# Kernel optimization log

Hardware: AMD Instinct MI355X
Metric: run time of the kernel (lower is better)

Reference implementation:

```python
import jax, jax.numpy as jnp
import numpy as np

IN_SIZE = 128
H_UNITS = 256
REC_MAX = min(25.0, 1.0 / float(np.sqrt(H_UNITS)))  # clip bound for recurrent kernels


def setup_inputs() -> dict:
    key = jax.random.key(0)
    ks = jax.random.split(key, 8)
    B, T, D, U = 64, 4096, IN_SIZE, H_UNITS
    xs = jax.random.normal(ks[0], (B, T, D), dtype=jnp.float32)
    # Original code inits input kernels/biases to zeros (degenerate); use small
    # random values so the baseline exercises nontrivial math (same formula).
    We = jax.random.normal(ks[1], (U, D), dtype=jnp.float32) * 0.02
    be = jnp.zeros((U,), dtype=jnp.float32)
    ue = jax.random.uniform(ks[2], (U,), minval=-REC_MAX, maxval=REC_MAX, dtype=jnp.float32)
    Wd = jax.random.normal(ks[3], (U, D), dtype=jnp.float32) * 0.02
    bd = jnp.zeros((U,), dtype=jnp.float32)
    ud = jax.random.uniform(ks[4], (U,), minval=-REC_MAX, maxval=REC_MAX, dtype=jnp.float32)
    lim = 1.0 / float(np.sqrt(U))  # torch.nn.Linear default init bound
    Wo = jax.random.uniform(ks[5], (D, U), minval=-lim, maxval=lim, dtype=jnp.float32)
    bo = jax.random.uniform(ks[6], (D,), minval=-lim, maxval=lim, dtype=jnp.float32)
    return {"xs": xs, "We": We, "be": be, "ue": ue, "Wd": Wd, "bd": bd, "ud": ud, "Wo": Wo, "bo": bo}


def reference(xs, We, be, ue, Wd, bd, ud, Wo, bo):
    B, T, D = xs.shape
    ue_c = jnp.clip(ue, -REC_MAX, REC_MAX)
    ud_c = jnp.clip(ud, -REC_MAX, REC_MAX)
    # IndRNN.forward never updates self.h, so the encoder hidden state is zeros
    # at every timestep; the encoder loop reduces to its last iteration:
    h = jax.nn.relu(xs[:, -1] @ We.T + be + ue_c * 0.0)  # [B, U]
    # ys[0]: readout of the (fixed) decoder hidden state
    out0 = h @ Wo.T + bo  # [B, D]
    loss = (xs[:, -1] - out0) ** 2  # [B, D]
    # train_step: decoder h stays fixed at encoder h for every timestep ->
    # all T-1 steps vectorize over time.
    dec_h = jax.nn.relu(jnp.einsum('btd,ud->btu', xs[:, 1:], Wd) + bd + ud_c * h[:, None, :])  # [B,T-1,U]
    outs = jnp.einsum('btu,du->btd', dec_h, Wo) + bo  # [B,T-1,D]
    loss = loss + jnp.sum((xs[:, :-1] - outs) ** 2, axis=1)  # sum over reversed(range(1,T))
    loss = loss / T
    return jnp.sum(loss) / B
```

## Files before the change

### kernel.cpp

```cpp
#include <hip/hip_runtime.h>

#define T_LEN 4096
#define D_IN 128
#define U_H 256
#define REC_MAXV 0.0625f

typedef __attribute__((ext_vector_type(4))) float f32x4;
typedef __attribute__((ext_vector_type(16))) float f32x16;
typedef __attribute__((ext_vector_type(2))) int int2v;
typedef long long i64;

template <bool HI>
__device__ __forceinline__ int pk8(float a, float b, int old) {
    return __builtin_amdgcn_cvt_pk_fp8_f32(a, b, old, HI);
}

__device__ __forceinline__ int reord32(int u) {
    int r = u & 31;
    return ((u >> 5) << 5) + (((r >> 2) & 1) << 4) + ((r >> 3) << 2) + (r & 3);
}

__global__ void k_pre(const float* __restrict__ xs, const float* __restrict__ We,
                      const float* __restrict__ be, const float* __restrict__ Wd,
                      const float* __restrict__ bd, const float* __restrict__ ud,
                      const float* __restrict__ Wo, const float* __restrict__ bo,
                      float* __restrict__ budR, float* __restrict__ boR,
                      char* __restrict__ WF8, float* __restrict__ part2) {
    __shared__ __align__(16) float hL[256];
    __shared__ float red[2];
    const int b = blockIdx.x, u = threadIdx.x;

    const f32x4* xr = (const f32x4*)(xs + ((size_t)b * T_LEN + (T_LEN - 1)) * D_IN);
    const f32x4* wr = (const f32x4*)(We + (size_t)u * D_IN);
    float s = 0.f;
#pragma unroll
    for (int i = 0; i < 32; ++i) {
        f32x4 a = xr[i], w = wr[i];
        s += a[0]*w[0] + a[1]*w[1] + a[2]*w[2] + a[3]*w[3];
    }
    s += be[u];
    s = fmaxf(s, 0.f);
    hL[u] = s;

    float udc = fminf(fmaxf(ud[u], -REC_MAXV), REC_MAXV);
    budR[(b << 8) + reord32(u)] = bd[u] + udc * s;

    if (b == 0 && u < 128) boR[reord32(u)] = bo[u];

    int gid = b * 256 + u;
    if (gid < 4096) {
        int f = gid >> 6, l = gid & 63;
        int ut = f >> 3, ks = f & 7;
        const float* src = Wd + (size_t)(ut * 32 + (l & 31)) * D_IN + ks * 16 + (l >> 5) * 8;
        int lo = pk8<false>(src[0], src[1], 0); lo = pk8<true>(src[2], src[3], lo);
        int hh = pk8<false>(src[4], src[5], 0); hh = pk8<true>(src[6], src[7], hh);
        *(int2v*)(WF8 + (size_t)gid * 8) = (int2v){lo, hh};
    } else if (gid < 8192) {
        int g = gid - 4096;
        int f = g >> 6, l = g & 63;
        int uk = f >> 2, dt = f & 3;
        const float* src = Wo + (size_t)(dt * 32 + (l & 31)) * U_H + uk * 16 + (l >> 5) * 8;
        int lo = pk8<false>(src[0], src[1], 0); lo = pk8<true>(src[2], src[3], lo);
        int hh = pk8<false>(src[4], src[5], 0); hh = pk8<true>(src[6], src[7], hh);
        *(int2v*)(WF8 + 32768 + (size_t)g * 8) = (int2v){lo, hh};
    }
    __syncthreads();

    float v = 0.f;
    if (u < 128) {
        const f32x4* hr = (const f32x4*)hL;
        const f32x4* wo = (const f32x4*)(Wo + (size_t)u * U_H);
        float s2 = 0.f;
#pragma unroll
        for (int i = 0; i < 64; ++i) {
            f32x4 a = hr[i], w = wo[i];
            s2 += a[0]*w[0] + a[1]*w[1] + a[2]*w[2] + a[3]*w[3];
        }
        s2 += bo[u];
        float x = xs[((size_t)b * T_LEN + T_LEN - 1) * D_IN + u];
        float diff = x - s2;
        v = diff * diff;
    }
#pragma unroll
    for (int o = 32; o > 0; o >>= 1) v += __shfl_down(v, o);
    if (u == 0) red[0] = v;
    if (u == 64) red[1] = v;
    __syncthreads();
    if (u == 0) part2[b] = red[0] + red[1];
}

__global__ __launch_bounds__(512, 2) void k_main(
        const float* __restrict__ xs, const float* __restrict__ budR,
        const float* __restrict__ boR, const char* __restrict__ WF8,
        float* __restrict__ part) {
    __shared__ __align__(16) char lds[67200];
    const int tid = threadIdx.x;

    for (int i = tid; i < 4096; i += 512)
        ((f32x4*)lds)[i] = ((const f32x4*)WF8)[i];
    const int b = blockIdx.x >> 4;
    if (tid < 64) ((f32x4*)(lds + 65536))[tid] = ((const f32x4*)(budR + b * 256))[tid];
    else if (tid < 96) ((f32x4*)(lds + 66560))[tid - 64] = ((const f32x4*)boR)[tid - 64];
    __syncthreads();

    const int wave = tid >> 6, lane = tid & 63;
    const int m = lane & 31, hi = lane >> 5;
    const float* xsb = xs + ((size_t)b << 19);
    const float* budL = (const float*)(lds + 65536);
    const float* boL  = (const float*)(lds + 66560);
    float* wsumf = (float*)(lds + 67072);

    const int tile = blockIdx.x * 8 + wave;
    const int t0 = (tile & 127) << 5;

    const float* xrow = xsb + (size_t)(t0 + m) * 128 + hi * 8;
    i64 x0, x1, x2, x3, x4, x5, x6, x7;
    {
#define LDX(KS, XV)                                                      \
        {   f32x4 v0 = *(const f32x4*)(xrow + KS * 16);                  \
            f32x4 v1 = *(const f32x4*)(xrow + KS * 16 + 4);              \
            int lo = pk8<false>(v0[0], v0[1], 0); lo = pk8<true>(v0[2], v0[3], lo); \
            int hh = pk8<false>(v1[0], v1[1], 0); hh = pk8<true>(v1[2], v1[3], hh); \
            XV = __builtin_bit_cast(i64, (int2v){lo, hh}); }
        LDX(0, x0) LDX(1, x1) LDX(2, x2) LDX(3, x3)
        LDX(4, x4) LDX(5, x5) LDX(6, x6) LDX(7, x7)
#undef LDX
    }

    f32x16 o0, o1, o2, o3;
#define OINIT(OV, DT)                                                    \
    {   const float* bp = boL + (DT) * 32 + hi * 16;                     \
        f32x4 b0 = *(const f32x4*)(bp), b1 = *(const f32x4*)(bp + 4);    \
        f32x4 b2 = *(const f32x4*)(bp + 8), b3 = *(const f32x4*)(bp + 12); \
        OV[0]=b0[0]; OV[1]=b0[1]; OV[2]=b0[2]; OV[3]=b0[3];              \
        OV[4]=b1[0]; OV[5]=b1[1]; OV[6]=b1[2]; OV[7]=b1[3];              \
        OV[8]=b2[0]; OV[9]=b2[1]; OV[10]=b2[2]; OV[11]=b2[3];            \
        OV[12]=b3[0]; OV[13]=b3[1]; OV[14]=b3[2]; OV[15]=b3[3]; }
    OINIT(o0, 0) OINIT(o1, 1) OINIT(o2, 2) OINIT(o3, 3)
#undef OINIT

#pragma clang loop unroll(disable)
    for (int ut = 0; ut < 8; ++ut) {
        f32x16 ca, cb;
        {
            const float* bp = budL + ut * 32 + hi * 16;
            f32x4 b0 = *(const f32x4*)(bp), b1 = *(const f32x4*)(bp + 4);
            f32x4 b2 = *(const f32x4*)(bp + 8), b3 = *(const f32x4*)(bp + 12);
            ca[0]=b0[0]; ca[1]=b0[1]; ca[2]=b0[2]; ca[3]=b0[3];
            ca[4]=b1[0]; ca[5]=b1[1]; ca[6]=b1[2]; ca[7]=b1[3];
            ca[8]=b2[0]; ca[9]=b2[1]; ca[10]=b2[2]; ca[11]=b2[3];
            ca[12]=b3[0]; ca[13]=b3[1]; ca[14]=b3[2]; ca[15]=b3[3];
#pragma unroll
            for (int i = 0; i < 16; ++i) cb[i] = 0.f;
        }
        const char* wb = lds + ((ut * 8) << 9) + (lane << 3);
        ca = __builtin_amdgcn_mfma_f32_32x32x16_fp8_fp8(*(const i64*)(wb + 0*512), x0, ca, 0,0,0);
        cb = __builtin_amdgcn_mfma_f32_32x32x16_fp8_fp8(*(const i64*)(wb + 1*512), x1, cb, 0,0,0);
        ca = __builtin_amdgcn_mfma_f32_32x32x16_fp8_fp8(*(const i64*)(wb + 2*512), x2, ca, 0,0,0);
        cb = __builtin_amdgcn_mfma_f32_32x32x16_fp8_fp8(*(const i64*)(wb + 3*512), x3, cb, 0,0,0);
        ca = __builtin_amdgcn_mfma_f32_32x32x16_fp8_fp8(*(const i64*)(wb + 4*512), x4, ca, 0,0,0);
        cb = __builtin_amdgcn_mfma_f32_32x32x16_fp8_fp8(*(const i64*)(wb + 5*512), x5, cb, 0,0,0);
        ca = __builtin_amdgcn_mfma_f32_32x32x16_fp8_fp8(*(const i64*)(wb + 6*512), x6, ca, 0,0,0);
        cb = __builtin_amdgcn_mfma_f32_32x32x16_fp8_fp8(*(const i64*)(wb + 7*512), x7, cb, 0,0,0);

        i64 dlo, dhi;
        {
            f32x16 c;
#pragma unroll
            for (int i = 0; i < 16; ++i) c[i] = fmaxf(ca[i] + cb[i], 0.f);
            int d0 = pk8<false>(c[0],  c[1],  0); d0 = pk8<true>(c[2],  c[3],  d0);
            int d1 = pk8<false>(c[4],  c[5],  0); d1 = pk8<true>(c[6],  c[7],  d1);
            int d2 = pk8<false>(c[8],  c[9],  0); d2 = pk8<true>(c[10], c[11], d2);
            int d3 = pk8<false>(c[12], c[13], 0); d3 = pk8<true>(c[14], c[15], d3);
            int2v s = __builtin_amdgcn_permlane32_swap(d0, d1, false, false);
            int2v t = __builtin_amdgcn_permlane32_swap(d2, d3, false, false);
            dlo = __builtin_bit_cast(i64, s);
            dhi = __builtin_bit_cast(i64, t);
        }

        const char* w2 = lds + 32768 + ((ut * 8) << 9) + (lane << 3);
        o0 = __builtin_amdgcn_mfma_f32_32x32x16_fp8_fp8(*(const i64*)(w2 + 0*512), dlo, o0, 0,0,0);
        o1 = __builtin_amdgcn_mfma_f32_32x32x16_fp8_fp8(*(const i64*)(w2 + 1*512), dlo, o1, 0,0,0);
        o2 = __builtin_amdgcn_mfma_f32_32x32x16_fp8_fp8(*(const i64*)(w2 + 2*512), dlo, o2, 0,0,0);
        o3 = __builtin_amdgcn_mfma_f32_32x32x16_fp8_fp8(*(const i64*)(w2 + 3*512), dlo, o3, 0,0,0);
        o0 = __builtin_amdgcn_mfma_f32_32x32x16_fp8_fp8(*(const i64*)(w2 + 4*512), dhi, o0, 0,0,0);
        o1 = __builtin_amdgcn_mfma_f32_32x32x16_fp8_fp8(*(const i64*)(w2 + 5*512), dhi, o1, 0,0,0);
        o2 = __builtin_amdgcn_mfma_f32_32x32x16_fp8_fp8(*(const i64*)(w2 + 6*512), dhi, o2, 0,0,0);
        o3 = __builtin_amdgcn_mfma_f32_32x32x16_fp8_fp8(*(const i64*)(w2 + 7*512), dhi, o3, 0,0,0);
    }

    const int t = t0 + m;
    const float sel = (t > 0) ? 1.f : 0.f;
    const float* trow = xsb + (size_t)((t > 0) ? t - 1 : 0) * 128;
    float lacc = 0.f;
#define EPI(OV, DT)                                                      \
    {   _Pragma("unroll")                                                \
        for (int q = 0; q < 4; ++q) {                                    \
            f32x4 tg = *(const f32x4*)(trow + (DT) * 32 + q * 8 + hi * 4); \
            _Pragma("unroll")                                            \
            for (int j = 0; j < 4; ++j) {                                \
                float diff = tg[j] - OV[q * 4 + j];                      \
                lacc += sel * diff * diff;                               \
            }                                                            \
        }                                                                \
    }
    EPI(o0, 0) EPI(o1, 1) EPI(o2, 2) EPI(o3, 3)
#undef EPI

#pragma unroll
    for (int o = 32; o > 0; o >>= 1) lacc += __shfl_down(lacc, o);
    if (lane == 0) wsumf[wave] = lacc;
    __syncthreads();
    if (tid == 0) {
        float s = 0.f;
#pragma unroll
        for (int i = 0; i < 8; ++i) s += wsumf[i];
        part[blockIdx.x] = s;
    }
}

__global__ void k_final(const float* __restrict__ part, const float* __restrict__ part2,
                        float* __restrict__ loss) {
    __shared__ float ws[16];
    const int tid = threadIdx.x;
    float v = part[tid];
    if (tid < 64) v += part2[tid];
#pragma unroll
    for (int o = 32; o > 0; o >>= 1) v += __shfl_down(v, o);
    if ((tid & 63) == 0) ws[tid >> 6] = v;
    __syncthreads();
    if (tid == 0) {
        float s = 0.f;
#pragma unroll
        for (int i = 0; i < 16; ++i) s += ws[i];
        *loss = s * (1.f / 262144.f);
    }
}

extern "C" void kernel_launch(void* const* d_in, const int* in_sizes, int n_in,
                              void* d_out, int out_size, void* d_ws, size_t ws_size,
                              hipStream_t stream) {
    const float* xs = (const float*)d_in[0];
    const float* We = (const float*)d_in[1];
    const float* be = (const float*)d_in[2];
    const float* Wd = (const float*)d_in[4];
    const float* bd = (const float*)d_in[5];
    const float* ud = (const float*)d_in[6];
    const float* Wo = (const float*)d_in[7];
    const float* bo = (const float*)d_in[8];
    float* loss = (float*)d_out;

    char* ws = (char*)d_ws;
    float* budR  = (float*)(ws);
    char*  WF8   = (char*)(ws + 65536);
    float* boR   = (float*)(ws + 131072);
    float* part  = (float*)(ws + 131584);
    float* part2 = (float*)(ws + 135680);

    k_pre<<<64, 256, 0, stream>>>(xs, We, be, Wd, bd, ud, Wo, bo,
                                  budR, boR, WF8, part2);
    k_main<<<1024, 512, 0, stream>>>(xs, budR, boR, WF8, part);
    k_final<<<1, 1024, 0, stream>>>(part, part2, loss);
}
```

Baseline: 59.95 us.

## Fuse preprocessing and final reduction into main kernel with last-block atomic

Removes the separate preprocessing and final-reduction kernels. Every main block now recomputes its batch's encoder hidden state, bias vector and fp8 weight packing directly into LDS, and the last block to finish, found through an atomic counter, does the global sum. This drops two launches and the global-memory round trip for the packed weights. In exchange each of the 1024 blocks redundantly computes the encoder matvec and converts both weight matrices from fp32, which adds global reads and ALU work per block, and a memset launch is added to clear the counter.

```diff
diff --git a/kernel.cpp b/kernel.cpp
--- a/kernel.cpp
+++ b/kernel.cpp
@@ -20,97 +20,89 @@
     return ((u >> 5) << 5) + (((r >> 2) & 1) << 4) + ((r >> 3) << 2) + (r & 3);
 }
 
-__global__ void k_pre(const float* __restrict__ xs, const float* __restrict__ We,
-                      const float* __restrict__ be, const float* __restrict__ Wd,
-                      const float* __restrict__ bd, const float* __restrict__ ud,
-                      const float* __restrict__ Wo, const float* __restrict__ bo,
-                      float* __restrict__ budR, float* __restrict__ boR,
-                      char* __restrict__ WF8, float* __restrict__ part2) {
-    __shared__ __align__(16) float hL[256];
-    __shared__ float red[2];
-    const int b = blockIdx.x, u = threadIdx.x;
-
-    const f32x4* xr = (const f32x4*)(xs + ((size_t)b * T_LEN + (T_LEN - 1)) * D_IN);
-    const f32x4* wr = (const f32x4*)(We + (size_t)u * D_IN);
-    float s = 0.f;
-#pragma unroll
-    for (int i = 0; i < 32; ++i) {
-        f32x4 a = xr[i], w = wr[i];
-        s += a[0]*w[0] + a[1]*w[1] + a[2]*w[2] + a[3]*w[3];
-    }
-    s += be[u];
-    s = fmaxf(s, 0.f);
-    hL[u] = s;
-
-    float udc = fminf(fmaxf(ud[u], -REC_MAXV), REC_MAXV);
-    budR[(b << 8) + reord32(u)] = bd[u] + udc * s;
-
-    if (b == 0 && u < 128) boR[reord32(u)] = bo[u];
-
-    int gid = b * 256 + u;
-    if (gid < 4096) {
-        int f = gid >> 6, l = gid & 63;
-        int ut = f >> 3, ks = f & 7;
-        const float* src = Wd + (size_t)(ut * 32 + (l & 31)) * D_IN + ks * 16 + (l >> 5) * 8;
-        int lo = pk8<false>(src[0], src[1], 0); lo = pk8<true>(src[2], src[3], lo);
-        int hh = pk8<false>(src[4], src[5], 0); hh = pk8<true>(src[6], src[7], hh);
-        *(int2v*)(WF8 + (size_t)gid * 8) = (int2v){lo, hh};
-    } else if (gid < 8192) {
-        int g = gid - 4096;
-        int f = g >> 6, l = g & 63;
-        int uk = f >> 2, dt = f & 3;
-        const float* src = Wo + (size_t)(dt * 32 + (l & 31)) * U_H + uk * 16 + (l >> 5) * 8;
-        int lo = pk8<false>(src[0], src[1], 0); lo = pk8<true>(src[2], src[3], lo);
-        int hh = pk8<false>(src[4], src[5], 0); hh = pk8<true>(src[6], src[7], hh);
-        *(int2v*)(WF8 + 32768 + (size_t)g * 8) = (int2v){lo, hh};
-    }
-    __syncthreads();
-
-    float v = 0.f;
-    if (u < 128) {
-        const f32x4* hr = (const f32x4*)hL;
-        const f32x4* wo = (const f32x4*)(Wo + (size_t)u * U_H);
-        float s2 = 0.f;
-#pragma unroll
-        for (int i = 0; i < 64; ++i) {
-            f32x4 a = hr[i], w = wo[i];
-            s2 += a[0]*w[0] + a[1]*w[1] + a[2]*w[2] + a[3]*w[3];
-        }
-        s2 += bo[u];
-        float x = xs[((size_t)b * T_LEN + T_LEN - 1) * D_IN + u];
-        float diff = x - s2;
-        v = diff * diff;
-    }
-#pragma unroll
-    for (int o = 32; o > 0; o >>= 1) v += __shfl_down(v, o);
-    if (u == 0) red[0] = v;
-    if (u == 64) red[1] = v;
-    __syncthreads();
-    if (u == 0) part2[b] = red[0] + red[1];
-}
-
 __global__ __launch_bounds__(512, 2) void k_main(
-        const float* __restrict__ xs, const float* __restrict__ budR,
-        const float* __restrict__ boR, const char* __restrict__ WF8,
-        float* __restrict__ part) {
+        const float* __restrict__ xs, const float* __restrict__ We,
+        const float* __restrict__ be, const float* __restrict__ Wd,
+        const float* __restrict__ bd, const float* __restrict__ ud,
+        const float* __restrict__ Wo, const float* __restrict__ bo,
+        float* __restrict__ part, int* __restrict__ cnt,
+        float* __restrict__ loss) {
     __shared__ __align__(16) char lds[67200];
     const int tid = threadIdx.x;
-
-    for (int i = tid; i < 4096; i += 512)
-        ((f32x4*)lds)[i] = ((const f32x4*)WF8)[i];
-    const int b = blockIdx.x >> 4;
-    if (tid < 64) ((f32x4*)(lds + 65536))[tid] = ((const f32x4*)(budR + b * 256))[tid];
-    else if (tid < 96) ((f32x4*)(lds + 66560))[tid - 64] = ((const f32x4*)boR)[tid - 64];
-    __syncthreads();
+    const int bid = blockIdx.x;
+    const int b = bid >> 4;
+    float* budL = (float*)(lds + 65536);
+    float* boL  = (float*)(lds + 66560);
+    float* wsumf = (float*)(lds + 67072);
+    int*   lflag = (int*)(lds + 67104);
+
+    float lacc = 0.f;
+
+    {
+        float* hL = (float*)lds;
+        if (tid < 256) {
+            const f32x4* xr = (const f32x4*)(xs + ((size_t)b * T_LEN + (T_LEN - 1)) * D_IN);
+            const f32x4* wr = (const f32x4*)(We + (size_t)tid * D_IN);
+            float s = 0.f;
+#pragma unroll
+            for (int i = 0; i < 32; ++i) {
+                f32x4 a = xr[i], w = wr[i];
+                s += a[0]*w[0] + a[1]*w[1] + a[2]*w[2] + a[3]*w[3];
+            }
+            s += be[tid];
+            s = fmaxf(s, 0.f);
+            hL[tid] = s;
+            float udc = fminf(fmaxf(ud[tid], -REC_MAXV), REC_MAXV);
+            budL[reord32(tid)] = bd[tid] + udc * s;
+        } else if (tid < 384) {
+            boL[reord32(tid - 256)] = bo[tid - 256];
+        }
+        __syncthreads();
+
+        if ((bid & 15) == 0 && tid < 128) {
+            const f32x4* hr = (const f32x4*)hL;
+            const f32x4* wo = (const f32x4*)(Wo + (size_t)tid * U_H);
+            float s2 = 0.f;
+#pragma unroll
+            for (int i = 0; i < 64; ++i) {
+                f32x4 a = hr[i], w = wo[i];
+                s2 += a[0]*w[0] + a[1]*w[1] + a[2]*w[2] + a[3]*w[3];
+            }
+            s2 += bo[tid];
+            float x = xs[((size_t)b * T_LEN + T_LEN - 1) * D_IN + tid];
+            float diff = x - s2;
+            lacc += diff * diff;
+        }
+        __syncthreads();
+
+#pragma clang loop unroll(disable)
+        for (int k = 0; k < 16; ++k) {
+            int gid = tid + (k << 9);
+            if (gid < 4096) {
+                int f = gid >> 6, l = gid & 63;
+                int ut = f >> 3, ks = f & 7;
+                const float* src = Wd + (size_t)(ut * 32 + (l & 31)) * D_IN + ks * 16 + (l >> 5) * 8;
+                int lo = pk8<false>(src[0], src[1], 0); lo = pk8<true>(src[2], src[3], lo);
+                int hh = pk8<false>(src[4], src[5], 0); hh = pk8<true>(src[6], src[7], hh);
+                *(int2v*)(lds + (size_t)gid * 8) = (int2v){lo, hh};
+            } else {
+                int g = gid - 4096;
+                int f = g >> 6, l = g & 63;
+                int uk = f >> 2, dt = f & 3;
+                const float* src = Wo + (size_t)(dt * 32 + (l & 31)) * U_H + uk * 16 + (l >> 5) * 8;
+                int lo = pk8<false>(src[0], src[1], 0); lo = pk8<true>(src[2], src[3], lo);
+                int hh = pk8<false>(src[4], src[5], 0); hh = pk8<true>(src[6], src[7], hh);
+                *(int2v*)(lds + 32768 + (size_t)g * 8) = (int2v){lo, hh};
+            }
+        }
+        __syncthreads();
+    }
 
     const int wave = tid >> 6, lane = tid & 63;
     const int m = lane & 31, hi = lane >> 5;
     const float* xsb = xs + ((size_t)b << 19);
-    const float* budL = (const float*)(lds + 65536);
-    const float* boL  = (const float*)(lds + 66560);
-    float* wsumf = (float*)(lds + 67072);
-
-    const int tile = blockIdx.x * 8 + wave;
+
+    const int tile = bid * 8 + wave;
     const int t0 = (tile & 127) << 5;
 
     const float* xrow = xsb + (size_t)(t0 + m) * 128 + hi * 8;
@@ -192,7 +184,6 @@
     const int t = t0 + m;
     const float sel = (t > 0) ? 1.f : 0.f;
     const float* trow = xsb + (size_t)((t > 0) ? t - 1 : 0) * 128;
-    float lacc = 0.f;
 #define EPI(OV, DT)                                                      \
     {   _Pragma("unroll")                                                \
         for (int q = 0; q < 4; ++q) {                                    \
@@ -215,25 +206,25 @@
         float s = 0.f;
 #pragma unroll
         for (int i = 0; i < 8; ++i) s += wsumf[i];
-        part[blockIdx.x] = s;
-    }
-}
-
-__global__ void k_final(const float* __restrict__ part, const float* __restrict__ part2,
-                        float* __restrict__ loss) {
-    __shared__ float ws[16];
-    const int tid = threadIdx.x;
-    float v = part[tid];
-    if (tid < 64) v += part2[tid];
-#pragma unroll
-    for (int o = 32; o > 0; o >>= 1) v += __shfl_down(v, o);
-    if ((tid & 63) == 0) ws[tid >> 6] = v;
+        part[bid] = s;
+        __threadfence();
+        int old = atomicAdd(cnt, 1);
+        lflag[0] = (old == 1023) ? 1 : 0;
+    }
     __syncthreads();
-    if (tid == 0) {
-        float s = 0.f;
-#pragma unroll
-        for (int i = 0; i < 16; ++i) s += ws[i];
-        *loss = s * (1.f / 262144.f);
+    if (lflag[0]) {
+        __threadfence();
+        float v = part[tid] + part[tid + 512];
+#pragma unroll
+        for (int o = 32; o > 0; o >>= 1) v += __shfl_down(v, o);
+        if (lane == 0) wsumf[wave] = v;
+        __syncthreads();
+        if (tid == 0) {
+            float s = 0.f;
+#pragma unroll
+            for (int i = 0; i < 8; ++i) s += wsumf[i];
+            *loss = s * (1.f / 262144.f);
+        }
     }
 }
 
@@ -250,15 +241,11 @@
     const float* bo = (const float*)d_in[8];
     float* loss = (float*)d_out;
 
-    char* ws = (char*)d_ws;
-    float* budR  = (float*)(ws);
-    char*  WF8   = (char*)(ws + 65536);
-    float* boR   = (float*)(ws + 131072);
-    float* part  = (float*)(ws + 131584);
-    float* part2 = (float*)(ws + 135680);
-
-    k_pre<<<64, 256, 0, stream>>>(xs, We, be, Wd, bd, ud, Wo, bo,
-                                  budR, boR, WF8, part2);
-    k_main<<<1024, 512, 0, stream>>>(xs, budR, boR, WF8, part);
-    k_final<<<1, 1024, 0, stream>>>(part, part2, loss);
-}
+    char* wsb = (char*)d_ws;
+    float* part = (float*)(wsb);
+    int*   cnt  = (int*)(wsb + 4096);
+
+    hipMemsetAsync(cnt, 0, 4, stream);
+    k_main<<<1024, 512, 0, stream>>>(xs, We, be, Wd, bd, ud, Wo, bo,
+                                     part, cnt, loss);
+}
```

Result: slower. 120.7 us (+101.3%).

## Issue x loads before LDS staging and fuse final reduction via last-block atomic

Applied to the files above, without the earlier changes.

The main kernel now issues its global loads of the xs tile into registers before copying the FP8 weights and biases into LDS, so the x-fetch latency overlaps the LDS staging and barrier. The separate final-reduction kernel is removed: each block bumps a global counter after writing its partial sum, and the last block to arrive reduces all partials and writes the loss. This saves one kernel launch but adds a memset, an atomic and thread fences, and holds 64 extra live registers per thread during staging, which may pressure occupancy.

```diff
diff --git a/kernel.cpp b/kernel.cpp
--- a/kernel.cpp
+++ b/kernel.cpp
@@ -92,40 +92,48 @@
 __global__ __launch_bounds__(512, 2) void k_main(
         const float* __restrict__ xs, const float* __restrict__ budR,
         const float* __restrict__ boR, const char* __restrict__ WF8,
-        float* __restrict__ part) {
+        const float* __restrict__ part2, float* __restrict__ part,
+        int* __restrict__ cnt, float* __restrict__ loss) {
     __shared__ __align__(16) char lds[67200];
     const int tid = threadIdx.x;
-
-    for (int i = tid; i < 4096; i += 512)
-        ((f32x4*)lds)[i] = ((const f32x4*)WF8)[i];
-    const int b = blockIdx.x >> 4;
-    if (tid < 64) ((f32x4*)(lds + 65536))[tid] = ((const f32x4*)(budR + b * 256))[tid];
-    else if (tid < 96) ((f32x4*)(lds + 66560))[tid - 64] = ((const f32x4*)boR)[tid - 64];
-    __syncthreads();
+    const int bid = blockIdx.x;
+    const int b = bid >> 4;
+    float* wsumf = (float*)(lds + 67072);
+    int*   lflag = (int*)(lds + 67104);
 
     const int wave = tid >> 6, lane = tid & 63;
     const int m = lane & 31, hi = lane >> 5;
     const float* xsb = xs + ((size_t)b << 19);
+    const int tile = bid * 8 + wave;
+    const int t0 = (tile & 127) << 5;
+
+    const float* xrow = xsb + (size_t)(t0 + m) * 128 + hi * 8;
+    f32x4 r0  = *(const f32x4*)(xrow +   0), r1  = *(const f32x4*)(xrow +   4);
+    f32x4 r2  = *(const f32x4*)(xrow +  16), r3  = *(const f32x4*)(xrow +  20);
+    f32x4 r4  = *(const f32x4*)(xrow +  32), r5  = *(const f32x4*)(xrow +  36);
+    f32x4 r6  = *(const f32x4*)(xrow +  48), r7  = *(const f32x4*)(xrow +  52);
+    f32x4 r8  = *(const f32x4*)(xrow +  64), r9  = *(const f32x4*)(xrow +  68);
+    f32x4 r10 = *(const f32x4*)(xrow +  80), r11 = *(const f32x4*)(xrow +  84);
+    f32x4 r12 = *(const f32x4*)(xrow +  96), r13 = *(const f32x4*)(xrow + 100);
+    f32x4 r14 = *(const f32x4*)(xrow + 112), r15 = *(const f32x4*)(xrow + 116);
+
+    for (int i = tid; i < 4096; i += 512)
+        ((f32x4*)lds)[i] = ((const f32x4*)WF8)[i];
+    if (tid < 64) ((f32x4*)(lds + 65536))[tid] = ((const f32x4*)(budR + b * 256))[tid];
+    else if (tid < 96) ((f32x4*)(lds + 66560))[tid - 64] = ((const f32x4*)boR)[tid - 64];
+    __syncthreads();
+
     const float* budL = (const float*)(lds + 65536);
     const float* boL  = (const float*)(lds + 66560);
-    float* wsumf = (float*)(lds + 67072);
-
-    const int tile = blockIdx.x * 8 + wave;
-    const int t0 = (tile & 127) << 5;
-
-    const float* xrow = xsb + (size_t)(t0 + m) * 128 + hi * 8;
+
     i64 x0, x1, x2, x3, x4, x5, x6, x7;
-    {
-#define LDX(KS, XV)                                                      \
-        {   f32x4 v0 = *(const f32x4*)(xrow + KS * 16);                  \
-            f32x4 v1 = *(const f32x4*)(xrow + KS * 16 + 4);              \
-            int lo = pk8<false>(v0[0], v0[1], 0); lo = pk8<true>(v0[2], v0[3], lo); \
-            int hh = pk8<false>(v1[0], v1[1], 0); hh = pk8<true>(v1[2], v1[3], hh); \
-            XV = __builtin_bit_cast(i64, (int2v){lo, hh}); }
-        LDX(0, x0) LDX(1, x1) LDX(2, x2) LDX(3, x3)
-        LDX(4, x4) LDX(5, x5) LDX(6, x6) LDX(7, x7)
-#undef LDX
-    }
+#define CV(V0, V1, XV)                                                   \
+    {   int lo = pk8<false>(V0[0], V0[1], 0); lo = pk8<true>(V0[2], V0[3], lo); \
+        int hh = pk8<false>(V1[0], V1[1], 0); hh = pk8<true>(V1[2], V1[3], hh); \
+        XV = __builtin_bit_cast(i64, (int2v){lo, hh}); }
+    CV(r0,  r1,  x0) CV(r2,  r3,  x1) CV(r4,  r5,  x2) CV(r6,  r7,  x3)
+    CV(r8,  r9,  x4) CV(r10, r11, x5) CV(r12, r13, x6) CV(r14, r15, x7)
+#undef CV
 
     f32x16 o0, o1, o2, o3;
 #define OINIT(OV, DT)                                                    \
@@ -215,25 +223,26 @@
         float s = 0.f;
 #pragma unroll
         for (int i = 0; i < 8; ++i) s += wsumf[i];
-        part[blockIdx.x] = s;
-    }
-}
-
-__global__ void k_final(const float* __restrict__ part, const float* __restrict__ part2,
-                        float* __restrict__ loss) {
-    __shared__ float ws[16];
-    const int tid = threadIdx.x;
-    float v = part[tid];
-    if (tid < 64) v += part2[tid];
-#pragma unroll
-    for (int o = 32; o > 0; o >>= 1) v += __shfl_down(v, o);
-    if ((tid & 63) == 0) ws[tid >> 6] = v;
-    __syncthreads();
-    if (tid == 0) {
-        float s = 0.f;
-#pragma unroll
-        for (int i = 0; i < 16; ++i) s += ws[i];
-        *loss = s * (1.f / 262144.f);
+        part[bid] = s;
+        __threadfence();
+        int old = atomicAdd(cnt, 1);
+        lflag[0] = (old == 1023) ? 1 : 0;
+    }
+    __syncthreads();
+    if (lflag[0]) {
+        __threadfence();
+        float v = part[tid] + part[tid + 512];
+        if (tid < 64) v += part2[tid];
+#pragma unroll
+        for (int o = 32; o > 0; o >>= 1) v += __shfl_down(v, o);
+        if (lane == 0) wsumf[wave] = v;
+        __syncthreads();
+        if (tid == 0) {
+            float s = 0.f;
+#pragma unroll
+            for (int i = 0; i < 8; ++i) s += wsumf[i];
+            *loss = s * (1.f / 262144.f);
+        }
     }
 }
 
@@ -250,15 +259,16 @@
     const float* bo = (const float*)d_in[8];
     float* loss = (float*)d_out;
 
-    char* ws = (char*)d_ws;
-    float* budR  = (float*)(ws);
-    char*  WF8   = (char*)(ws + 65536);
-    float* boR   = (float*)(ws + 131072);
-    float* part  = (float*)(ws + 131584);
-    float* part2 = (float*)(ws + 135680);
-
+    char* wsb = (char*)d_ws;
+    float* budR  = (float*)(wsb);
+    char*  WF8   = (char*)(wsb + 65536);
+    float* boR   = (float*)(wsb + 131072);
+    float* part  = (float*)(wsb + 131584);
+    float* part2 = (float*)(wsb + 135680);
+    int*   cnt   = (int*)(wsb + 135936);
+
+    hipMemsetAsync(cnt, 0, 4, stream);
     k_pre<<<64, 256, 0, stream>>>(xs, We, be, Wd, bd, ud, Wo, bo,
                                   budR, boR, WF8, part2);
-    k_main<<<1024, 512, 0, stream>>>(xs, budR, boR, WF8, part);
-    k_final<<<1, 1024, 0, stream>>>(part, part2, loss);
-}
+    k_main<<<1024, 512, 0, stream>>>(xs, budR, boR, WF8, part2, part, cnt, loss);
+}
```

Measured after the change: 95.44 us. 1.59x slower.

## Switch to scaled 32x32x64 FP8 MFMA with repacked weight fragments

Applied to the files above, without the earlier changes.

Replaces the 32x32x16 FP8 MFMA chain with the MI355X scaled 32x32x64 f8f6f4 MFMA at unit scale, so each instruction covers four times the K depth. Weight packing in the pre-kernel and the x fragment loading are reorganised to match the wider operand layout. The hidden tile is now recombined across lane halves with permlane32 swaps and selects so it can feed the second GEMM. The intent is to issue far fewer MFMA instructions per tile, in exchange for more LDS loads per fragment and extra register pressure from 8-dword operands.

```diff
diff --git a/kernel.cpp b/kernel.cpp
--- a/kernel.cpp
+++ b/kernel.cpp
@@ -4,11 +4,12 @@
 #define D_IN 128
 #define U_H 256
 #define REC_MAXV 0.0625f
+#define SC1 0x7F7F7F7F
 
 typedef __attribute__((ext_vector_type(4))) float f32x4;
 typedef __attribute__((ext_vector_type(16))) float f32x16;
 typedef __attribute__((ext_vector_type(2))) int int2v;
-typedef long long i64;
+typedef __attribute__((ext_vector_type(8))) int int8v;
 
 template <bool HI>
 __device__ __forceinline__ int pk8(float a, float b, int old) {
@@ -48,21 +49,21 @@
     if (b == 0 && u < 128) boR[reord32(u)] = bo[u];
 
     int gid = b * 256 + u;
-    if (gid < 4096) {
-        int f = gid >> 6, l = gid & 63;
-        int ut = f >> 3, ks = f & 7;
-        const float* src = Wd + (size_t)(ut * 32 + (l & 31)) * D_IN + ks * 16 + (l >> 5) * 8;
-        int lo = pk8<false>(src[0], src[1], 0); lo = pk8<true>(src[2], src[3], lo);
-        int hh = pk8<false>(src[4], src[5], 0); hh = pk8<true>(src[6], src[7], hh);
-        *(int2v*)(WF8 + (size_t)gid * 8) = (int2v){lo, hh};
-    } else if (gid < 8192) {
-        int g = gid - 4096;
-        int f = g >> 6, l = g & 63;
-        int uk = f >> 2, dt = f & 3;
-        const float* src = Wo + (size_t)(dt * 32 + (l & 31)) * U_H + uk * 16 + (l >> 5) * 8;
-        int lo = pk8<false>(src[0], src[1], 0); lo = pk8<true>(src[2], src[3], lo);
-        int hh = pk8<false>(src[4], src[5], 0); hh = pk8<true>(src[6], src[7], hh);
-        *(int2v*)(WF8 + 32768 + (size_t)g * 8) = (int2v){lo, hh};
+    if (gid < 8192) {
+        int f = gid >> 9, l = (gid >> 3) & 63, r = gid & 7;
+        int uw = f >> 1, w = f & 1;
+        const float* src = Wd + (size_t)(uw * 32 + (l & 31)) * D_IN
+                              + w * 64 + (l >> 5) * 32 + r * 4;
+        int v = pk8<false>(src[0], src[1], 0); v = pk8<true>(src[2], src[3], v);
+        *(int*)(WF8 + ((size_t)f << 11) + ((r >> 1) << 9) + (l << 3) + ((r & 1) << 2)) = v;
+    } else {
+        int g = gid - 8192;
+        int f = g >> 9, l = (g >> 3) & 63, r = g & 7;
+        int dw = f >> 2, uwin = f & 3;
+        const float* src = Wo + (size_t)(dw * 32 + (l & 31)) * U_H
+                              + uwin * 64 + (l >> 5) * 32 + r * 4;
+        int v = pk8<false>(src[0], src[1], 0); v = pk8<true>(src[2], src[3], v);
+        *(int*)(WF8 + 32768 + ((size_t)f << 11) + ((r >> 1) << 9) + (l << 3) + ((r & 1) << 2)) = v;
     }
     __syncthreads();
 
@@ -89,6 +90,49 @@
     if (u == 0) part2[b] = red[0] + red[1];
 }
 
+__device__ __forceinline__ int8v ldfrag(const char* p) {
+    int2v t0 = *(const int2v*)(p);
+    int2v t1 = *(const int2v*)(p + 512);
+    int2v t2 = *(const int2v*)(p + 1024);
+    int2v t3 = *(const int2v*)(p + 1536);
+    int8v a;
+    a[0] = t0[0]; a[1] = t0[1]; a[2] = t1[0]; a[3] = t1[1];
+    a[4] = t2[0]; a[5] = t2[1]; a[6] = t3[0]; a[7] = t3[1];
+    return a;
+}
+
+__device__ __forceinline__ int8v ph1s(const char* lds, const float* budL,
+                                      int lane, int hi, int uw,
+                                      int8v xw0, int8v xw1) {
+    f32x16 c;
+    {
+        const float* bp = budL + uw * 32 + hi * 16;
+        f32x4 b0 = *(const f32x4*)(bp), b1 = *(const f32x4*)(bp + 4);
+        f32x4 b2 = *(const f32x4*)(bp + 8), b3 = *(const f32x4*)(bp + 12);
+        c[0]=b0[0]; c[1]=b0[1]; c[2]=b0[2]; c[3]=b0[3];
+        c[4]=b1[0]; c[5]=b1[1]; c[6]=b1[2]; c[7]=b1[3];
+        c[8]=b2[0]; c[9]=b2[1]; c[10]=b2[2]; c[11]=b2[3];
+        c[12]=b3[0]; c[13]=b3[1]; c[14]=b3[2]; c[15]=b3[3];
+    }
+    int8v a0 = ldfrag(lds + ((size_t)(uw * 2 + 0) << 11) + (lane << 3));
+    int8v a1 = ldfrag(lds + ((size_t)(uw * 2 + 1) << 11) + (lane << 3));
+    c = __builtin_amdgcn_mfma_scale_f32_32x32x64_f8f6f4(a0, xw0, c, 0, 0, 0, SC1, 0, SC1);
+    c = __builtin_amdgcn_mfma_scale_f32_32x32x64_f8f6f4(a1, xw1, c, 0, 0, 0, SC1, 0, SC1);
+#pragma unroll
+    for (int i = 0; i < 16; ++i) c[i] = fmaxf(c[i], 0.f);
+    int8v p;
+#pragma unroll
+    for (int q = 0; q < 4; ++q) {
+        int own = pk8<false>(c[4*q], c[4*q+1], 0);
+        own = pk8<true>(c[4*q+2], c[4*q+3], own);
+        int2v sw = __builtin_amdgcn_permlane32_swap(own, own, false, false);
+        int partner = hi ? sw[0] : sw[1];
+        p[2*q]     = hi ? partner : own;
+        p[2*q + 1] = hi ? own : partner;
+    }
+    return p;
+}
+
 __global__ __launch_bounds__(512, 2) void k_main(
         const float* __restrict__ xs, const float* __restrict__ budR,
         const float* __restrict__ boR, const char* __restrict__ WF8,
@@ -113,18 +157,16 @@
     const int tile = blockIdx.x * 8 + wave;
     const int t0 = (tile & 127) << 5;
 
-    const float* xrow = xsb + (size_t)(t0 + m) * 128 + hi * 8;
-    i64 x0, x1, x2, x3, x4, x5, x6, x7;
-    {
-#define LDX(KS, XV)                                                      \
-        {   f32x4 v0 = *(const f32x4*)(xrow + KS * 16);                  \
-            f32x4 v1 = *(const f32x4*)(xrow + KS * 16 + 4);              \
-            int lo = pk8<false>(v0[0], v0[1], 0); lo = pk8<true>(v0[2], v0[3], lo); \
-            int hh = pk8<false>(v1[0], v1[1], 0); hh = pk8<true>(v1[2], v1[3], hh); \
-            XV = __builtin_bit_cast(i64, (int2v){lo, hh}); }
-        LDX(0, x0) LDX(1, x1) LDX(2, x2) LDX(3, x3)
-        LDX(4, x4) LDX(5, x5) LDX(6, x6) LDX(7, x7)
-#undef LDX
+    const float* xb0 = xsb + (size_t)(t0 + m) * 128 + hi * 32;
+    int8v xw0, xw1;
+#pragma unroll
+    for (int r = 0; r < 8; ++r) {
+        f32x4 v0 = *(const f32x4*)(xb0 + r * 4);
+        int t = pk8<false>(v0[0], v0[1], 0); t = pk8<true>(v0[2], v0[3], t);
+        xw0[r] = t;
+        f32x4 v1 = *(const f32x4*)(xb0 + 64 + r * 4);
+        int t2 = pk8<false>(v1[0], v1[1], 0); t2 = pk8<true>(v1[2], v1[3], t2);
+        xw1[r] = t2;
     }
 
     f32x16 o0, o1, o2, o3;
@@ -140,53 +182,21 @@
 #undef OINIT
 
 #pragma clang loop unroll(disable)
-    for (int ut = 0; ut < 8; ++ut) {
-        f32x16 ca, cb;
-        {
-            const float* bp = budL + ut * 32 + hi * 16;
-            f32x4 b0 = *(const f32x4*)(bp), b1 = *(const f32x4*)(bp + 4);
-            f32x4 b2 = *(const f32x4*)(bp + 8), b3 = *(const f32x4*)(bp + 12);
-            ca[0]=b0[0]; ca[1]=b0[1]; ca[2]=b0[2]; ca[3]=b0[3];
-            ca[4]=b1[0]; ca[5]=b1[1]; ca[6]=b1[2]; ca[7]=b1[3];
-            ca[8]=b2[0]; ca[9]=b2[1]; ca[10]=b2[2]; ca[11]=b2[3];
-            ca[12]=b3[0]; ca[13]=b3[1]; ca[14]=b3[2]; ca[15]=b3[3];
-#pragma unroll
-            for (int i = 0; i < 16; ++i) cb[i] = 0.f;
-        }
-        const char* wb = lds + ((ut * 8) << 9) + (lane << 3);
-        ca = __builtin_amdgcn_mfma_f32_32x32x16_fp8_fp8(*(const i64*)(wb + 0*512), x0, ca, 0,0,0);
-        cb = __builtin_amdgcn_mfma_f32_32x32x16_fp8_fp8(*(const i64*)(wb + 1*512), x1, cb, 0,0,0);
-        ca = __builtin_amdgcn_mfma_f32_32x32x16_fp8_fp8(*(const i64*)(wb + 2*512), x2, ca, 0,0,0);
-        cb = __builtin_amdgcn_mfma_f32_32x32x16_fp8_fp8(*(const i64*)(wb + 3*512), x3, cb, 0,0,0);
-        ca = __builtin_amdgcn_mfma_f32_32x32x16_fp8_fp8(*(const i64*)(wb + 4*512), x4, ca, 0,0,0);
-        cb = __builtin_amdgcn_mfma_f32_32x32x16_fp8_fp8(*(const i64*)(wb + 5*512), x5, cb, 0,0,0);
-        ca = __builtin_amdgcn_mfma_f32_32x32x16_fp8_fp8(*(const i64*)(wb + 6*512), x6, ca, 0,0,0);
-        cb = __builtin_amdgcn_mfma_f32_32x32x16_fp8_fp8(*(const i64*)(wb + 7*512), x7, cb, 0,0,0);
-
-        i64 dlo, dhi;
-        {
-            f32x16 c;
-#pragma unroll
-            for (int i = 0; i < 16; ++i) c[i] = fmaxf(ca[i] + cb[i], 0.f);
-            int d0 = pk8<false>(c[0],  c[1],  0); d0 = pk8<true>(c[2],  c[3],  d0);
-            int d1 = pk8<false>(c[4],  c[5],  0); d1 = pk8<true>(c[6],  c[7],  d1);
-            int d2 = pk8<false>(c[8],  c[9],  0); d2 = pk8<true>(c[10], c[11], d2);
-            int d3 = pk8<false>(c[12], c[13], 0); d3 = pk8<true>(c[14], c[15], d3);
-            int2v s = __builtin_amdgcn_permlane32_swap(d0, d1, false, false);
-            int2v t = __builtin_amdgcn_permlane32_swap(d2, d3, false, false);
-            dlo = __builtin_bit_cast(i64, s);
-            dhi = __builtin_bit_cast(i64, t);
-        }
-
-        const char* w2 = lds + 32768 + ((ut * 8) << 9) + (lane << 3);
-        o0 = __builtin_amdgcn_mfma_f32_32x32x16_fp8_fp8(*(const i64*)(w2 + 0*512), dlo, o0, 0,0,0);
-        o1 = __builtin_amdgcn_mfma_f32_32x32x16_fp8_fp8(*(const i64*)(w2 + 1*512), dlo, o1, 0,0,0);
-        o2 = __builtin_amdgcn_mfma_f32_32x32x16_fp8_fp8(*(const i64*)(w2 + 2*512), dlo, o2, 0,0,0);
-        o3 = __builtin_amdgcn_mfma_f32_32x32x16_fp8_fp8(*(const i64*)(w2 + 3*512), dlo, o3, 0,0,0);
-        o0 = __builtin_amdgcn_mfma_f32_32x32x16_fp8_fp8(*(const i64*)(w2 + 4*512), dhi, o0, 0,0,0);
-        o1 = __builtin_amdgcn_mfma_f32_32x32x16_fp8_fp8(*(const i64*)(w2 + 5*512), dhi, o1, 0,0,0);
-        o2 = __builtin_amdgcn_mfma_f32_32x32x16_fp8_fp8(*(const i64*)(w2 + 6*512), dhi, o2, 0,0,0);
-        o3 = __builtin_amdgcn_mfma_f32_32x32x16_fp8_fp8(*(const i64*)(w2 + 7*512), dhi, o3, 0,0,0);
+    for (int pr = 0; pr < 4; ++pr) {
+        int8v ep = ph1s(lds, budL, lane, hi, 2 * pr, xw0, xw1);
+        int8v op = ph1s(lds, budL, lane, hi, 2 * pr + 1, xw0, xw1);
+        int8v decR;
+#pragma unroll
+        for (int r = 0; r < 8; ++r) decR[r] = hi ? op[r] : ep[r];
+        const char* wo2 = lds + 32768 + (lane << 3);
+        int8v w0 = ldfrag(wo2 + ((size_t)(0 * 4 + pr) << 11));
+        int8v w1 = ldfrag(wo2 + ((size_t)(1 * 4 + pr) << 11));
+        int8v w2 = ldfrag(wo2 + ((size_t)(2 * 4 + pr) << 11));
+        int8v w3 = ldfrag(wo2 + ((size_t)(3 * 4 + pr) << 11));
+        o0 = __builtin_amdgcn_mfma_scale_f32_32x32x64_f8f6f4(w0, decR, o0, 0, 0, 0, SC1, 0, SC1);
+        o1 = __builtin_amdgcn_mfma_scale_f32_32x32x64_f8f6f4(w1, decR, o1, 0, 0, 0, SC1, 0, SC1);
+        o2 = __builtin_amdgcn_mfma_scale_f32_32x32x64_f8f6f4(w2, decR, o2, 0, 0, 0, SC1, 0, SC1);
+        o3 = __builtin_amdgcn_mfma_scale_f32_32x32x64_f8f6f4(w3, decR, o3, 0, 0, 0, SC1, 0, SC1);
     }
 
     const int t = t0 + m;
```

Result: slower. 63.80 us (+6.4%).
